# Kernel tuning notes

Hardware: AMD Instinct MI355X
Metric: run time of the kernel (lower is better)

Reference implementation:

```python
import jax, jax.numpy as jnp
import numpy as np

B, S, C, D, SN = 32, 145, 768, 8192, 64

def setup_inputs() -> dict:
    key = jax.random.key(0)
    ks = jax.random.split(key, 12)
    h1 = jax.random.randint(ks[0], (C,), 0, D, dtype=jnp.int32)
    h2 = jax.random.randint(ks[1], (C,), 0, D, dtype=jnp.int32)
    s1 = jax.random.randint(ks[2], (C,), 0, 2, dtype=jnp.int32) * 2 - 1
    s2 = jax.random.randint(ks[3], (C,), 0, 2, dtype=jnp.int32) * 2 - 1
    return {
        'sensor': jax.random.normal(ks[4], (B, 1, SN), jnp.float32),
        'image_embeds': jax.random.normal(ks[5], (B, S, C), jnp.float32),
        'image_masks': jnp.ones((B, S), jnp.int32),
        'h1': h1, 'h2': h2, 's1': s1, 's2': s2,
        'd': D,
        'W_sensor': jax.random.normal(ks[6], (C, SN), jnp.float32) * 0.02,
        'b_sensor': jnp.zeros((C,), jnp.float32),
        'W_s2': jax.random.normal(ks[7], (S, 1), jnp.float32) * 0.02,
        'b_s2': jnp.zeros((S,), jnp.float32),
        'W_out': jax.random.normal(ks[8], (1, S), jnp.float32) * 0.02,
        'b_out': jnp.zeros((1,), jnp.float32),
        'tok_emb': jax.random.normal(ks[9], (2, C), jnp.float32) * 0.02,
    }

def _sketch(x, h, s, d):
    # count-sketch: scatter c channels into d bins with random signs
    v = x * s.astype(x.dtype)                      # [B,S,C]
    Q = jnp.zeros(x.shape[:2] + (d,), x.dtype)
    return Q.at[:, :, h].add(v)                    # duplicate hash indices accumulate

def _tsp(x, h1, h2, s1, s2, d):
    # FFT circular convolution of the two sketches
    F1 = jnp.fft.fft(_sketch(x, h1, s1, d))
    F2 = jnp.fft.fft(_sketch(x, h2, s2, d))
    return jnp.fft.ifft(F1 * F2).real              # [B,S,d]

def reference(sensor, image_embeds, image_masks, h1, h2, s1, s2, d,
              W_sensor, b_sensor, W_s2, b_s2, W_out, b_out, tok_emb):
    # sensor branch: [B,1,SN] -> [B,1,C] -> [B,C,1] -> [B,C,145] -> [B,145,C]
    se = sensor @ W_sensor.T + b_sensor
    se = jnp.swapaxes(se, 1, 2)
    se = se @ W_s2.T + b_s2
    se = jnp.swapaxes(se, 1, 2)
    # image branch: add token-type embedding (idx=1), masks define shape only
    img = image_embeds + tok_emb[1][None, None, :]
    z_x = _tsp(img, h1, h2, s1, s2, d)
    z_y = _tsp(se, h1, h2, s1, s2, d)
    ip = jnp.sum(z_x * z_y, axis=2)                # [B,S]
    bp = jnp.sign(ip) * jnp.sqrt(jnp.abs(ip) + 1e-5)
    norm = jnp.maximum(jnp.linalg.norm(bp, axis=1, keepdims=True), 1e-12)
    bp = bp / norm                                 # F.normalize p=2 dim=1
    out = bp @ W_out.T + b_out                     # [B,1]
    return out
```

## Files before the change

### kernel.cpp

```cpp
#include <hip/hip_runtime.h>
#include <hip/hip_bf16.h>
#include <math.h>

#define DD 8192
#define CC 768
#define SS 145
#define BB 32
#define SN 64
#define SROWS 160
#define NCKA 24

#define NETD 12
#define NCH 12
#define M01W 36
#define NWGD (BB*2*NETD)

#define ZT 512
#define NSL 16

typedef __attribute__((ext_vector_type(8))) short short8;
typedef __attribute__((ext_vector_type(4))) float f32x4;

__device__ __forceinline__ void gload16(const void* g, void* l) {
    __builtin_amdgcn_global_load_lds(
        (const __attribute__((address_space(1))) unsigned int*)g,
        (__attribute__((address_space(3))) unsigned int*)l, 16, 0, 0);
}

__global__ __launch_bounds__(512) void kS(
    const float* __restrict__ sensor, const float* __restrict__ Wsen,
    const float* __restrict__ bsen,
    const int* __restrict__ h1, const int* __restrict__ h2,
    const int* __restrict__ s1, const int* __restrict__ s2,
    float4* __restrict__ CTG, float2* __restrict__ P2G)
{
    __shared__ float2 P2l[DD];
    __shared__ float  sens[SN];
    const int b   = blockIdx.x;
    const int tid = threadIdx.x;

    if (tid < SN) sens[tid] = sensor[b*SN + tid];
    {
        float4* p4 = (float4*)P2l;
        #pragma unroll
        for (int i = 0; i < 8; ++i) p4[tid + i*512] = make_float4(0.f,0.f,0.f,0.f);
    }
    __syncthreads();

    for (int c = tid; c < CC; c += 512) {
        float u = bsen[c];
        const float4* w = (const float4*)(Wsen + (size_t)c*SN);
        #pragma unroll
        for (int n4 = 0; n4 < 16; ++n4) {
            float4 wv = w[n4];
            u += sens[4*n4+0]*wv.x + sens[4*n4+1]*wv.y
               + sens[4*n4+2]*wv.z + sens[4*n4+3]*wv.w;
        }
        float f1 = (float)s1[c], f2 = (float)s2[c];
        float4 ct;
        ct.x = u * f1; ct.y = f1; ct.z = __int_as_float(h1[c]); ct.w = 0.f;
        CTG[(size_t)b*CC + c] = ct;
        int t = h2[c];
        unsafeAtomicAdd(&P2l[t].x, u * f2);
        unsafeAtomicAdd(&P2l[t].y, f2);
    }
    __syncthreads();

    {
        const float4* p4 = (const float4*)P2l;
        float4* dst = (float4*)(P2G + (size_t)b*DD);
        #pragma unroll
        for (int i = 0; i < 8; ++i) dst[tid + i*512] = p4[tid + i*512];
    }
}

__global__ __launch_bounds__(ZT) void kZ(
    const float4* __restrict__ CTG, const float2* __restrict__ P2G,
    unsigned int* __restrict__ ZP, unsigned short* __restrict__ Z11b)
{
    __shared__ float2 P2l[DD];

    const int bid = blockIdx.x;
    const int wg  = (bid & 7)*(BB*NSL/8) + (bid >> 3);
    const int b   = wg >> 4;
    const int dsl = wg & (NSL-1);
    const int tid = threadIdx.x;

    {
        const float4* src = (const float4*)(P2G + (size_t)b*DD);
        float4* dst = (float4*)P2l;
        #pragma unroll
        for (int i = 0; i < 8; ++i) dst[tid + i*ZT] = src[tid + i*ZT];
    }
    __syncthreads();

    const int d = dsl*ZT + tid;
    const float4* ctp = CTG + (size_t)b*CC;
    float accU = 0.f, accC = 0.f, acc1 = 0.f;
    #pragma unroll 4
    for (int c = 0; c < CC; ++c) {
        float4 ct = ctp[c];
        int idx = (d - __float_as_int(ct.z)) & (DD-1);
        float2 p = P2l[idx];
        accU = fmaf(ct.x, p.x, accU);
        accC = fmaf(ct.x, p.y, fmaf(ct.y, p.x, accC));
        acc1 = fmaf(ct.y, p.y, acc1);
    }

    __hip_bfloat16 zu = __float2bfloat16(accU);
    __hip_bfloat16 zc = __float2bfloat16(accC);
    ZP[(size_t)b*DD + d] = (unsigned int)*(unsigned short*)&zu
                         | ((unsigned int)*(unsigned short*)&zc << 16);
    if (b == 0) {
        __hip_bfloat16 z1 = __float2bfloat16(acc1);
        Z11b[d] = *(unsigned short*)&z1;
    }
}

__global__ __launch_bounds__(384) void kA(
    const float* __restrict__ E, const float* __restrict__ tok,
    const int* __restrict__ s1, unsigned int* __restrict__ A1u)
{
    const int b  = blockIdx.x;
    const int r0 = blockIdx.y * 16;
    const int p  = threadIdx.x;
    const int c  = 2*p;
    const int ck = p >> 4;
    const int c2 = p & 15;
    const float s1a = (float)s1[c], s1b = (float)s1[c+1];
    const float ta = tok[CC + c] * s1a, tb = tok[CC + c + 1] * s1b;
    #pragma unroll
    for (int rr = 0; rr < 16; ++rr) {
        int row = r0 + rr;
        unsigned int word = 0;
        if (row < SS) {
            float2 ev = *(const float2*)&E[((size_t)b*SS + row)*CC + c];
            __hip_bfloat16 x0 = __float2bfloat16(ev.x*s1a + ta);
            __hip_bfloat16 x1 = __float2bfloat16(ev.y*s1b + tb);
            word = (unsigned int)*(unsigned short*)&x0
                 | ((unsigned int)*(unsigned short*)&x1 << 16);
        }
        int gp = (c2 >> 2) ^ (row & 3);
        A1u[((size_t)(b*NCKA + ck)*SROWS + row)*16 + gp*4 + (c2 & 3)] = word;
    }
}

__global__ __launch_bounds__(512) void kM11(
    const unsigned short* __restrict__ Z11b,
    const int* __restrict__ h1, const int* __restrict__ h2,
    unsigned int* __restrict__ M11u)
{
    __shared__ unsigned short Z11l[DD];
    const int ck  = blockIdx.x;
    const int tid = threadIdx.x;
    {
        const uint4* src = (const uint4*)Z11b;
        uint4* dst = (uint4*)Z11l;
        #pragma unroll
        for (int i = 0; i < 2; ++i) dst[tid + i*512] = src[tid + i*512];
    }
    __syncthreads();

    const int hA = h1[ck*32 + 2*(tid & 15)];
    const int hB = h1[ck*32 + 2*(tid & 15) + 1];
    const int cp = tid & 15;
    #pragma unroll 4
    for (int i = 0; i < 24; ++i) {
        int idx = tid + i*512;
        int ep  = idx >> 4;
        int cpp = idx & 15;
        int ha = (cpp == cp) ? hA : h1[ck*32 + 2*cpp];
        int hb = (cpp == cp) ? hB : h1[ck*32 + 2*cpp + 1];
        int he = h2[ep];
        unsigned int lo = Z11l[(ha + he) & (DD-1)];
        unsigned int hi = Z11l[(hb + he) & (DD-1)];
        M11u[((size_t)ck*768 + ep)*16 + cpp] = lo | (hi << 16);
    }
}

__global__ __launch_bounds__(512, 4) void kD(
    const unsigned int* __restrict__ A1u,
    const unsigned short* __restrict__ M11,
    const float* __restrict__ E, const float* __restrict__ tok,
    const int* __restrict__ h1, const int* __restrict__ h2,
    const int* __restrict__ s2,
    const float* __restrict__ Ws2, const float* __restrict__ bs2,
    const unsigned int* __restrict__ ZP, float* __restrict__ Q)
{
    __shared__ __align__(16) unsigned int   ZPl[DD];
    __shared__ __align__(16) unsigned short Lt[2][SROWS*32];
    __shared__ __align__(16) unsigned int   Mt01[2][64*M01W];
    __shared__ unsigned short h1l[CC];

    const int bid = blockIdx.x;
    const int wg  = (bid & 7)*(NWGD/8) + (bid >> 3);
    const int b   = wg / 24;
    const int r   = wg % 24;
    const int ch  = r / 12;
    const int et  = r % 12;
    const int tid = threadIdx.x;
    const int e0  = et * 64;
    const int cb0 = ch * 384;

    {
        const uint4* src = (const uint4*)(ZP + (size_t)b*DD);
        uint4* dst = (uint4*)ZPl;
        #pragma unroll
        for (int i = 0; i < 4; ++i) dst[tid + i*512] = src[tid + i*512];
    }
    for (int c = tid; c < CC; c += 512) h1l[c] = (unsigned short)h1[c];

    const int lane = tid & 63;
    const int wv   = tid >> 6;
    const int esub = wv & 3;
    const int shf  = wv >> 2;
    const int l15  = lane & 15;
    const int l4   = lane >> 4;
    const int eg   = e0 + esub*16 + l15;

    int gh2[4];
    #pragma unroll
    for (int j = 0; j < 4; ++j) gh2[j] = h2[e0 + ((tid + j*512) >> 5)];
    __syncthreads();

    const char* Abase = (const char*)A1u + (size_t)b*NCKA*SROWS*64;

#define STAGE_A(K, BUF) { \
    const char* cbase = Abase + (size_t)(ch*NCH + (K))*SROWS*64; \
    gload16(cbase + wv*1024 + lane*16, (char*)(BUF) + wv*1024); \
    if (wv < 2) \
        gload16(cbase + 8192 + wv*1024 + lane*16, \
                (char*)(BUF) + 8192 + wv*1024); \
    }

#define GATHER(K, MT) { \
    _Pragma("unroll") \
    for (int j = 0; j < 4; ++j) { \
        int idx = tid + j*512; \
        int ge = idx >> 5, gc = idx & 31; \
        int ad = ((int)h1l[cb0 + (K)*32 + gc] + gh2[j]) & (DD-1); \
        MT[ge*M01W + gc] = ZPl[ad]; \
    } }

#define LOADB2(K) \
    (*(const short8*)&M11[((size_t)(ch*NCH + (K))*768 + eg)*32 + l4*8])

#define MFMA_STEP(LT, MT, BQ) { \
    const unsigned int* mp = &MT[(esub*16 + l15)*M01W + l4*8]; \
    uint4 p0 = *(const uint4*)mp; \
    uint4 p1 = *(const uint4*)(mp + 4); \
    union { unsigned int u[4]; short8 s; } b0, b1; \
    b0.u[0] = (p0.x & 0xffffu) | (p0.y << 16); \
    b1.u[0] = (p0.x >> 16)     | (p0.y & 0xffff0000u); \
    b0.u[1] = (p0.z & 0xffffu) | (p0.w << 16); \
    b1.u[1] = (p0.z >> 16)     | (p0.w & 0xffff0000u); \
    b0.u[2] = (p1.x & 0xffffu) | (p1.y << 16); \
    b1.u[2] = (p1.x >> 16)     | (p1.y & 0xffff0000u); \
    b0.u[3] = (p1.z & 0xffffu) | (p1.w << 16); \
    b1.u[3] = (p1.z >> 16)     | (p1.w & 0xffff0000u); \
    _Pragma("unroll") \
    for (int t = 0; t < 5; ++t) { \
        int R = shf*80 + t*16 + l15; \
        short8 af = *(const short8*)&LT[R*32 + ((l4 ^ (R & 3))*8)]; \
        acc0[t] = __builtin_amdgcn_mfma_f32_16x16x32_bf16(af, b0.s, acc0[t], 0,0,0); \
        acc1[t] = __builtin_amdgcn_mfma_f32_16x16x32_bf16(af, b1.s, acc1[t], 0,0,0); \
        acc2[t] = __builtin_amdgcn_mfma_f32_16x16x32_bf16(af, BQ,   acc2[t], 0,0,0); \
    } }

    f32x4 acc0[5], acc1[5], acc2[5];
    #pragma unroll
    for (int t = 0; t < 5; ++t) {
        acc0[t] = (f32x4){0.f,0.f,0.f,0.f};
        acc1[t] = (f32x4){0.f,0.f,0.f,0.f};
        acc2[t] = (f32x4){0.f,0.f,0.f,0.f};
    }

    short8 bqA, bqB;
    STAGE_A(0, Lt[0])
    GATHER(0, Mt01[0])
    bqA = LOADB2(0);
    __syncthreads();

    #pragma unroll 1
    for (int k = 0; k < NCH; k += 2) {
        if (k + 1 < NCH) {
            STAGE_A(k + 1, Lt[1])
            GATHER(k + 1, Mt01[1])
            bqB = LOADB2(k + 1);
        }
        MFMA_STEP(Lt[0], Mt01[0], bqA)
        __syncthreads();

        if (k + 2 < NCH) {
            STAGE_A(k + 2, Lt[0])
            GATHER(k + 2, Mt01[0])
            bqA = LOADB2(k + 2);
        }
        if (k + 1 < NCH) {
            MFMA_STEP(Lt[1], Mt01[1], bqB)
        }
        __syncthreads();
    }
#undef STAGE_A
#undef GATHER
#undef LOADB2
#undef MFMA_STEP

    const float s2e = (float)s2[eg];
    const float t2e = tok[CC + eg] * s2e;
    #pragma unroll
    for (int t = 0; t < 5; ++t) {
        #pragma unroll
        for (int rr = 0; rr < 4; ++rr) {
            int s = shf*80 + t*16 + l4*4 + rr;
            float qv = 0.f;
            if (s < SS) {
                float a2v = E[((size_t)b*SS + s)*CC + eg] * s2e + t2e;
                float w2v = Ws2[s], bbv = bs2[s];
                qv = (w2v*w2v*acc0[t][rr] + w2v*bbv*acc1[t][rr]
                      + bbv*bbv*acc2[t][rr]) * a2v;
            }
            qv += __shfl_xor(qv, 1);
            qv += __shfl_xor(qv, 2);
            qv += __shfl_xor(qv, 4);
            qv += __shfl_xor(qv, 8);
            if (l15 == 0 && s < SS)
                unsafeAtomicAdd(&Q[b*SS + s], qv);
        }
    }
}

__global__ __launch_bounds__(256) void kE(
    const float* __restrict__ Q, const float* __restrict__ Wout,
    const float* __restrict__ bout, float* __restrict__ out)
{
    __shared__ float red[8];
    const int b = blockIdx.x, tid = threadIdx.x;
    float v = 0.f, w = 0.f;
    if (tid < SS) {
        float ip = Q[b*SS + tid];
        float sg = (ip > 0.f) ? 1.f : ((ip < 0.f) ? -1.f : 0.f);
        v = sg * sqrtf(fabsf(ip) + 1e-5f);
        w = v * Wout[tid];
    }
    float sq = v * v;
    #pragma unroll
    for (int off = 32; off > 0; off >>= 1) {
        sq += __shfl_down(sq, off, 64);
        w  += __shfl_down(w,  off, 64);
    }
    if ((tid & 63) == 0) { red[tid >> 6] = sq; red[4 + (tid >> 6)] = w; }
    __syncthreads();
    if (tid == 0) {
        float ssq  = red[0] + red[1] + red[2] + red[3];
        float sw   = red[4] + red[5] + red[6] + red[7];
        float norm = fmaxf(sqrtf(ssq), 1e-12f);
        out[b] = sw / norm + bout[0];
    }
}

extern "C" void kernel_launch(void* const* d_in, const int* in_sizes, int n_in,
                              void* d_out, int out_size, void* d_ws, size_t ws_size,
                              hipStream_t stream) {
    const float* sensor = (const float*)d_in[0];
    const float* E      = (const float*)d_in[1];
    const int*   h1     = (const int*)d_in[3];
    const int*   h2     = (const int*)d_in[4];
    const int*   s1     = (const int*)d_in[5];
    const int*   s2     = (const int*)d_in[6];
    const float* Wsen   = (const float*)d_in[8];
    const float* bsen   = (const float*)d_in[9];
    const float* Ws2    = (const float*)d_in[10];
    const float* bs2    = (const float*)d_in[11];
    const float* Wout   = (const float*)d_in[12];
    const float* bout   = (const float*)d_in[13];
    const float* tok    = (const float*)d_in[14];
    float* out = (float*)d_out;

    char* ws = (char*)d_ws;
    float4* CTG = (float4*)ws;
    float2* P2G = (float2*)(ws + (size_t)BB*CC*16);
    unsigned int* A1u = (unsigned int*)ws;
    const size_t A1_BYTES = (size_t)BB*NCKA*SROWS*64;
    unsigned int*   ZP   = (unsigned int*)(ws + A1_BYTES);
    unsigned short* Z11b = (unsigned short*)(ws + A1_BYTES + (size_t)BB*DD*4);
    unsigned int*   M11u = (unsigned int*)((char*)Z11b + (size_t)DD*2);
    float* Q = (float*)((char*)M11u + (size_t)NCKA*768*32*2);

    hipMemsetAsync(Q, 0, (size_t)BB*SS*sizeof(float), stream);

    kS<<<dim3(BB), dim3(512), 0, stream>>>(
        sensor, Wsen, bsen, h1, h2, s1, s2, CTG, P2G);

    kZ<<<dim3(BB*NSL), dim3(ZT), 0, stream>>>(CTG, P2G, ZP, Z11b);

    kA<<<dim3(BB, SROWS/16), dim3(384), 0, stream>>>(E, tok, s1, A1u);

    kM11<<<dim3(NCKA), dim3(512), 0, stream>>>(Z11b, h1, h2, M11u);

    kD<<<dim3(NWGD), dim3(512), 0, stream>>>(
        A1u, (const unsigned short*)M11u, E, tok, h1, h2, s2, Ws2, bs2, ZP, Q);

    kE<<<dim3(BB), dim3(256), 0, stream>>>(Q, Wout, bout, out);
}
```

Baseline: 170.9 us.

## Single-buffer kD staging tiles, add MFMA priority, skip unused Z11 accumulation

kD drops the double-buffered Lt/Mt01 shared tiles for single buffers and loads the next chunk only after the MFMA step, with an extra barrier per iteration. The aim is to cut shared-memory use so more workgroups fit per CU, giving up overlap of loads with MFMA inside a workgroup. MFMA sections are wrapped in s_setprio to favour the matrix work across waves. kZ now accumulates acc1 only for batch 0, where it is actually stored.

```diff
diff --git a/kernel.cpp b/kernel.cpp
--- a/kernel.cpp
+++ b/kernel.cpp
@@ -85,6 +85,7 @@
     const int b   = wg >> 4;
     const int dsl = wg & (NSL-1);
     const int tid = threadIdx.x;
+    const bool doZ11 = (b == 0);
 
     {
         const float4* src = (const float4*)(P2G + (size_t)b*DD);
@@ -104,14 +105,14 @@
         float2 p = P2l[idx];
         accU = fmaf(ct.x, p.x, accU);
         accC = fmaf(ct.x, p.y, fmaf(ct.y, p.x, accC));
-        acc1 = fmaf(ct.y, p.y, acc1);
+        if (doZ11) acc1 = fmaf(ct.y, p.y, acc1);
     }
 
     __hip_bfloat16 zu = __float2bfloat16(accU);
     __hip_bfloat16 zc = __float2bfloat16(accC);
     ZP[(size_t)b*DD + d] = (unsigned int)*(unsigned short*)&zu
                          | ((unsigned int)*(unsigned short*)&zc << 16);
-    if (b == 0) {
+    if (doZ11) {
         __hip_bfloat16 z1 = __float2bfloat16(acc1);
         Z11b[d] = *(unsigned short*)&z1;
     }
@@ -188,8 +189,8 @@
     const unsigned int* __restrict__ ZP, float* __restrict__ Q)
 {
     __shared__ __align__(16) unsigned int   ZPl[DD];
-    __shared__ __align__(16) unsigned short Lt[2][SROWS*32];
-    __shared__ __align__(16) unsigned int   Mt01[2][64*M01W];
+    __shared__ __align__(16) unsigned short Lt[SROWS*32];
+    __shared__ __align__(16) unsigned int   Mt01[64*M01W];
     __shared__ unsigned short h1l[CC];
 
     const int bid = blockIdx.x;
@@ -225,28 +226,28 @@
 
     const char* Abase = (const char*)A1u + (size_t)b*NCKA*SROWS*64;
 
-#define STAGE_A(K, BUF) { \
+#define STAGE_A(K) { \
     const char* cbase = Abase + (size_t)(ch*NCH + (K))*SROWS*64; \
-    gload16(cbase + wv*1024 + lane*16, (char*)(BUF) + wv*1024); \
+    gload16(cbase + wv*1024 + lane*16, (char*)Lt + wv*1024); \
     if (wv < 2) \
         gload16(cbase + 8192 + wv*1024 + lane*16, \
-                (char*)(BUF) + 8192 + wv*1024); \
-    }
-
-#define GATHER(K, MT) { \
+                (char*)Lt + 8192 + wv*1024); \
+    }
+
+#define GATHER(K) { \
     _Pragma("unroll") \
     for (int j = 0; j < 4; ++j) { \
         int idx = tid + j*512; \
         int ge = idx >> 5, gc = idx & 31; \
         int ad = ((int)h1l[cb0 + (K)*32 + gc] + gh2[j]) & (DD-1); \
-        MT[ge*M01W + gc] = ZPl[ad]; \
+        Mt01[ge*M01W + gc] = ZPl[ad]; \
     } }
 
 #define LOADB2(K) \
     (*(const short8*)&M11[((size_t)(ch*NCH + (K))*768 + eg)*32 + l4*8])
 
-#define MFMA_STEP(LT, MT, BQ) { \
-    const unsigned int* mp = &MT[(esub*16 + l15)*M01W + l4*8]; \
+#define MFMA_STEP(BQ) { \
+    const unsigned int* mp = &Mt01[(esub*16 + l15)*M01W + l4*8]; \
     uint4 p0 = *(const uint4*)mp; \
     uint4 p1 = *(const uint4*)(mp + 4); \
     union { unsigned int u[4]; short8 s; } b0, b1; \
@@ -258,14 +259,17 @@
     b1.u[2] = (p1.x >> 16)     | (p1.y & 0xffff0000u); \
     b0.u[3] = (p1.z & 0xffffu) | (p1.w << 16); \
     b1.u[3] = (p1.z >> 16)     | (p1.w & 0xffff0000u); \
+    __builtin_amdgcn_s_setprio(1); \
     _Pragma("unroll") \
     for (int t = 0; t < 5; ++t) { \
         int R = shf*80 + t*16 + l15; \
-        short8 af = *(const short8*)&LT[R*32 + ((l4 ^ (R & 3))*8)]; \
+        short8 af = *(const short8*)&Lt[R*32 + ((l4 ^ (R & 3))*8)]; \
         acc0[t] = __builtin_amdgcn_mfma_f32_16x16x32_bf16(af, b0.s, acc0[t], 0,0,0); \
         acc1[t] = __builtin_amdgcn_mfma_f32_16x16x32_bf16(af, b1.s, acc1[t], 0,0,0); \
         acc2[t] = __builtin_amdgcn_mfma_f32_16x16x32_bf16(af, BQ,   acc2[t], 0,0,0); \
-    } }
+    } \
+    __builtin_amdgcn_s_setprio(0); \
+    }
 
     f32x4 acc0[5], acc1[5], acc2[5];
     #pragma unroll
@@ -275,31 +279,22 @@
         acc2[t] = (f32x4){0.f,0.f,0.f,0.f};
     }
 
-    short8 bqA, bqB;
-    STAGE_A(0, Lt[0])
-    GATHER(0, Mt01[0])
-    bqA = LOADB2(0);
+    short8 bq;
+    STAGE_A(0)
+    GATHER(0)
+    bq = LOADB2(0);
     __syncthreads();
 
     #pragma unroll 1
-    for (int k = 0; k < NCH; k += 2) {
+    for (int k = 0; k < NCH; ++k) {
+        MFMA_STEP(bq)
+        __syncthreads();
         if (k + 1 < NCH) {
-            STAGE_A(k + 1, Lt[1])
-            GATHER(k + 1, Mt01[1])
-            bqB = LOADB2(k + 1);
+            STAGE_A(k + 1)
+            GATHER(k + 1)
+            bq = LOADB2(k + 1);
+            __syncthreads();
         }
-        MFMA_STEP(Lt[0], Mt01[0], bqA)
-        __syncthreads();
-
-        if (k + 2 < NCH) {
-            STAGE_A(k + 2, Lt[0])
-            GATHER(k + 2, Mt01[0])
-            bqA = LOADB2(k + 2);
-        }
-        if (k + 1 < NCH) {
-            MFMA_STEP(Lt[1], Mt01[1], bqB)
-        }
-        __syncthreads();
     }
 #undef STAGE_A
 #undef GATHER
```

After: 174.8 us. 1.02x slower.

## Split kZ channel loop across two half-blocks and merge kA with kM11

Applied to the files above, without the earlier changes.

kZ now runs 1024 threads per block: two groups of 512 each handle half of the 768 channels for the same d slice. Their partial sums are combined through shared memory, CT loads are batched eight at a time, and acc1 is computed only for batch 0. The image-prep kernel kA and the M11 gather kernel kM11 are merged into one launch of 344 blocks, which removes a kernel launch and lets the two independent jobs share the GPU. The costs are an extra block-wide barrier and reduction in kZ, and idle threads in the kA-role blocks of the merged kernel.

```diff
diff --git a/kernel.cpp b/kernel.cpp
--- a/kernel.cpp
+++ b/kernel.cpp
@@ -15,8 +15,8 @@
 #define M01W 36
 #define NWGD (BB*2*NETD)
 
-#define ZT 512
-#define NSL 16
+#define ZT2 1024
+#define NSL2 16
 
 typedef __attribute__((ext_vector_type(8))) short short8;
 typedef __attribute__((ext_vector_type(4))) float f32x4;
@@ -74,107 +74,121 @@
     }
 }
 
-__global__ __launch_bounds__(ZT) void kZ(
+__global__ __launch_bounds__(ZT2) void kZ(
     const float4* __restrict__ CTG, const float2* __restrict__ P2G,
     unsigned int* __restrict__ ZP, unsigned short* __restrict__ Z11b)
 {
     __shared__ float2 P2l[DD];
+    __shared__ float4 red[512];
 
     const int bid = blockIdx.x;
-    const int wg  = (bid & 7)*(BB*NSL/8) + (bid >> 3);
+    const int wg  = (bid & 7)*(BB*NSL2/8) + (bid >> 3);
     const int b   = wg >> 4;
-    const int dsl = wg & (NSL-1);
+    const int dsl = wg & 15;
     const int tid = threadIdx.x;
+    const int dt  = tid & 511;
+    const int ch  = tid >> 9;
+    const bool doZ11 = (b == 0);
 
     {
         const float4* src = (const float4*)(P2G + (size_t)b*DD);
         float4* dst = (float4*)P2l;
         #pragma unroll
-        for (int i = 0; i < 8; ++i) dst[tid + i*ZT] = src[tid + i*ZT];
-    }
-    __syncthreads();
-
-    const int d = dsl*ZT + tid;
-    const float4* ctp = CTG + (size_t)b*CC;
+        for (int i = 0; i < 4; ++i) dst[tid + i*ZT2] = src[tid + i*ZT2];
+    }
+    __syncthreads();
+
+    const int d = dsl*512 + dt;
+    const float4* ctp = CTG + (size_t)b*CC + ch*384;
     float accU = 0.f, accC = 0.f, acc1 = 0.f;
-    #pragma unroll 4
-    for (int c = 0; c < CC; ++c) {
-        float4 ct = ctp[c];
-        int idx = (d - __float_as_int(ct.z)) & (DD-1);
-        float2 p = P2l[idx];
-        accU = fmaf(ct.x, p.x, accU);
-        accC = fmaf(ct.x, p.y, fmaf(ct.y, p.x, accC));
-        acc1 = fmaf(ct.y, p.y, acc1);
-    }
-
-    __hip_bfloat16 zu = __float2bfloat16(accU);
-    __hip_bfloat16 zc = __float2bfloat16(accC);
-    ZP[(size_t)b*DD + d] = (unsigned int)*(unsigned short*)&zu
-                         | ((unsigned int)*(unsigned short*)&zc << 16);
-    if (b == 0) {
-        __hip_bfloat16 z1 = __float2bfloat16(acc1);
-        Z11b[d] = *(unsigned short*)&z1;
-    }
-}
-
-__global__ __launch_bounds__(384) void kA(
+    #pragma unroll 1
+    for (int cb = 0; cb < 384; cb += 8) {
+        float4 ct[8];
+        #pragma unroll
+        for (int j = 0; j < 8; ++j) ct[j] = ctp[cb + j];
+        #pragma unroll
+        for (int j = 0; j < 8; ++j) {
+            int idx = (d - __float_as_int(ct[j].z)) & (DD-1);
+            float2 p = P2l[idx];
+            accU = fmaf(ct[j].x, p.x, accU);
+            accC = fmaf(ct[j].x, p.y, fmaf(ct[j].y, p.x, accC));
+            if (doZ11) acc1 = fmaf(ct[j].y, p.y, acc1);
+        }
+    }
+
+    if (ch == 1) red[dt] = make_float4(accU, accC, acc1, 0.f);
+    __syncthreads();
+    if (ch == 0) {
+        float4 o = red[dt];
+        accU += o.x; accC += o.y; acc1 += o.z;
+        __hip_bfloat16 zu = __float2bfloat16(accU);
+        __hip_bfloat16 zc = __float2bfloat16(accC);
+        ZP[(size_t)b*DD + d] = (unsigned int)*(unsigned short*)&zu
+                             | ((unsigned int)*(unsigned short*)&zc << 16);
+        if (doZ11) {
+            __hip_bfloat16 z1 = __float2bfloat16(acc1);
+            Z11b[d] = *(unsigned short*)&z1;
+        }
+    }
+}
+
+__global__ __launch_bounds__(512) void kAM(
     const float* __restrict__ E, const float* __restrict__ tok,
-    const int* __restrict__ s1, unsigned int* __restrict__ A1u)
-{
-    const int b  = blockIdx.x;
-    const int r0 = blockIdx.y * 16;
-    const int p  = threadIdx.x;
-    const int c  = 2*p;
-    const int ck = p >> 4;
-    const int c2 = p & 15;
-    const float s1a = (float)s1[c], s1b = (float)s1[c+1];
-    const float ta = tok[CC + c] * s1a, tb = tok[CC + c + 1] * s1b;
-    #pragma unroll
-    for (int rr = 0; rr < 16; ++rr) {
-        int row = r0 + rr;
-        unsigned int word = 0;
-        if (row < SS) {
-            float2 ev = *(const float2*)&E[((size_t)b*SS + row)*CC + c];
-            __hip_bfloat16 x0 = __float2bfloat16(ev.x*s1a + ta);
-            __hip_bfloat16 x1 = __float2bfloat16(ev.y*s1b + tb);
-            word = (unsigned int)*(unsigned short*)&x0
-                 | ((unsigned int)*(unsigned short*)&x1 << 16);
-        }
-        int gp = (c2 >> 2) ^ (row & 3);
-        A1u[((size_t)(b*NCKA + ck)*SROWS + row)*16 + gp*4 + (c2 & 3)] = word;
-    }
-}
-
-__global__ __launch_bounds__(512) void kM11(
+    const int* __restrict__ s1, unsigned int* __restrict__ A1u,
     const unsigned short* __restrict__ Z11b,
     const int* __restrict__ h1, const int* __restrict__ h2,
     unsigned int* __restrict__ M11u)
 {
     __shared__ unsigned short Z11l[DD];
-    const int ck  = blockIdx.x;
+    const int bid = blockIdx.x;
     const int tid = threadIdx.x;
-    {
-        const uint4* src = (const uint4*)Z11b;
-        uint4* dst = (uint4*)Z11l;
-        #pragma unroll
-        for (int i = 0; i < 2; ++i) dst[tid + i*512] = src[tid + i*512];
-    }
-    __syncthreads();
-
-    const int hA = h1[ck*32 + 2*(tid & 15)];
-    const int hB = h1[ck*32 + 2*(tid & 15) + 1];
-    const int cp = tid & 15;
-    #pragma unroll 4
-    for (int i = 0; i < 24; ++i) {
-        int idx = tid + i*512;
-        int ep  = idx >> 4;
-        int cpp = idx & 15;
-        int ha = (cpp == cp) ? hA : h1[ck*32 + 2*cpp];
-        int hb = (cpp == cp) ? hB : h1[ck*32 + 2*cpp + 1];
-        int he = h2[ep];
-        unsigned int lo = Z11l[(ha + he) & (DD-1)];
-        unsigned int hi = Z11l[(hb + he) & (DD-1)];
-        M11u[((size_t)ck*768 + ep)*16 + cpp] = lo | (hi << 16);
+
+    if (bid < 320) {
+        if (tid < 384) {
+            const int b  = bid / 10;
+            const int r0 = (bid % 10) * 16;
+            const int c  = 2*tid;
+            const int ck = tid >> 4;
+            const int c2 = tid & 15;
+            const float s1a = (float)s1[c], s1b = (float)s1[c+1];
+            const float ta = tok[CC + c] * s1a, tb = tok[CC + c + 1] * s1b;
+            #pragma unroll
+            for (int rr = 0; rr < 16; ++rr) {
+                int row = r0 + rr;
+                unsigned int word = 0;
+                if (row < SS) {
+                    float2 ev = *(const float2*)&E[((size_t)b*SS + row)*CC + c];
+                    __hip_bfloat16 x0 = __float2bfloat16(ev.x*s1a + ta);
+                    __hip_bfloat16 x1 = __float2bfloat16(ev.y*s1b + tb);
+                    word = (unsigned int)*(unsigned short*)&x0
+                         | ((unsigned int)*(unsigned short*)&x1 << 16);
+                }
+                int gp = (c2 >> 2) ^ (row & 3);
+                A1u[((size_t)(b*NCKA + ck)*SROWS + row)*16 + gp*4 + (c2 & 3)] = word;
+            }
+        }
+    } else {
+        const int ck = bid - 320;
+        {
+            const uint4* src = (const uint4*)Z11b;
+            uint4* dst = (uint4*)Z11l;
+            #pragma unroll
+            for (int i = 0; i < 2; ++i) dst[tid + i*512] = src[tid + i*512];
+        }
+        __syncthreads();
+
+        #pragma unroll 4
+        for (int i = 0; i < 24; ++i) {
+            int idx = tid + i*512;
+            int ep  = idx >> 4;
+            int cpp = idx & 15;
+            int ha = h1[ck*32 + 2*cpp];
+            int hb = h1[ck*32 + 2*cpp + 1];
+            int he = h2[ep];
+            unsigned int lo = Z11l[(ha + he) & (DD-1)];
+            unsigned int hi = Z11l[(hb + he) & (DD-1)];
+            M11u[((size_t)ck*768 + ep)*16 + cpp] = lo | (hi << 16);
+        }
     }
 }
 
@@ -392,11 +406,10 @@
     kS<<<dim3(BB), dim3(512), 0, stream>>>(
         sensor, Wsen, bsen, h1, h2, s1, s2, CTG, P2G);
 
-    kZ<<<dim3(BB*NSL), dim3(ZT), 0, stream>>>(CTG, P2G, ZP, Z11b);
-
-    kA<<<dim3(BB, SROWS/16), dim3(384), 0, stream>>>(E, tok, s1, A1u);
-
-    kM11<<<dim3(NCKA), dim3(512), 0, stream>>>(Z11b, h1, h2, M11u);
+    kZ<<<dim3(BB*NSL2), dim3(ZT2), 0, stream>>>(CTG, P2G, ZP, Z11b);
+
+    kAM<<<dim3(344), dim3(512), 0, stream>>>(
+        E, tok, s1, A1u, Z11b, h1, h2, M11u);
 
     kD<<<dim3(NWGD), dim3(512), 0, stream>>>(
         A1u, (const unsigned short*)M11u, E, tok, h1, h2, s2, Ws2, bs2, ZP, Q);
```

Result: slower. 185.8 us (+8.7%).
